# Performance work log

Hardware: AMD Instinct MI355X
Metric: run time of the kernel (lower is better)

Reference implementation:

```python
import jax, jax.numpy as jnp
import numpy as np

B, T, I, H = 64, 512, 512, 1024

def setup_inputs() -> dict:
    key = jax.random.key(0)
    ks = jax.random.split(key, 12)
    s_i = 1.0 / np.sqrt(I)
    s_h = 1.0 / np.sqrt(H)
    inp = {
        'x': jax.random.normal(ks[0], (B, T, I), dtype=jnp.float32),
        'h0': jnp.zeros((B, H), dtype=jnp.float32),
        'Wz': jax.random.uniform(ks[1], (H, I), jnp.float32, -s_i, s_i),
        'bz': jax.random.uniform(ks[2], (H,), jnp.float32, -s_i, s_i),
        'Uz': jax.random.uniform(ks[3], (H, H), jnp.float32, -s_h, s_h),
        'Wr': jax.random.uniform(ks[4], (H, I), jnp.float32, -s_i, s_i),
        'br': jax.random.uniform(ks[5], (H,), jnp.float32, -s_i, s_i),
        'Ur': jax.random.uniform(ks[6], (H, H), jnp.float32, -s_h, s_h),
        'Wh': jax.random.uniform(ks[7], (H, I), jnp.float32, -s_i, s_i),
        'bh': jax.random.uniform(ks[8], (H,), jnp.float32, -s_i, s_i),
        'Uh': jax.random.uniform(ks[9], (H, H), jnp.float32, -s_h, s_h),
    }
    return inp

def reference(x, h0, Wz, bz, Uz, Wr, br, Ur, Wh, bh, Uh):
    # Precompute all input projections for every timestep in 3 big GEMMs
    xz = jnp.einsum('bti,hi->bth', x, Wz) + bz  # [B,T,H]
    xr = jnp.einsum('bti,hi->bth', x, Wr) + br
    xh = jnp.einsum('bti,hi->bth', x, Wh) + bh
    # scan over time (recurrence)
    xs = (jnp.swapaxes(xz, 0, 1), jnp.swapaxes(xr, 0, 1), jnp.swapaxes(xh, 0, 1))  # [T,B,H]

    def step(h, inp):
        xz_t, xr_t, xh_t = inp
        z = jax.nn.sigmoid(xz_t + h @ Uz.T)
        r = jax.nn.sigmoid(xr_t + h @ Ur.T)
        h_tilde = jnp.tanh(xh_t + (r * h) @ Uh.T)
        h_new = (1.0 - z) * h + z * h_tilde
        return h_new, h_new

    h_last, outs = jax.lax.scan(step, h0, xs)  # outs: [T,B,H]
    outputs = jnp.swapaxes(outs, 0, 1)  # [B,T,H]
    return outputs, h_last
```

## Files before the change

kernel.cpp:

```cpp
#include <hip/hip_runtime.h>
#include <hip/hip_bf16.h>
#include <stdint.h>


#define B_ 64
#define T_ 512
#define I_ 512
#define H_ 1024

typedef __attribute__((ext_vector_type(4))) float f32x4;
typedef __attribute__((ext_vector_type(8))) short s16x8;

__device__ __forceinline__ unsigned short f2bf(float f) {
  union { float f; uint32_t u; } v; v.f = f;
  uint32_t u = v.u;
  u += 0x7fffu + ((u >> 16) & 1u);
  return (unsigned short)(u >> 16);
}
__device__ __forceinline__ float bf2f(unsigned short h) {
  union { uint32_t u; float f; } v; v.u = ((uint32_t)h) << 16;
  return v.f;
}

__global__ void k_split(const float* __restrict__ src, uint16_t* __restrict__ dst,
                        int kshift, int total) {
  int K = 1 << kshift;
  for (int i = blockIdx.x * blockDim.x + threadIdx.x; i < total;
       i += gridDim.x * blockDim.x) {
    int n = i >> kshift, k = i & (K - 1);
    float f = src[i];
    unsigned short hi = f2bf(f);
    unsigned short lo = f2bf(f - bf2f(hi));
    size_t base = (size_t)n * (3 * K);
    dst[base + k] = hi;
    dst[base + K + k] = lo;
    dst[base + 2 * K + k] = hi;
  }
}

__global__ void k_init(const float* __restrict__ h0, float* __restrict__ h,
                       uint16_t* __restrict__ h2) {
  for (int i = blockIdx.x * blockDim.x + threadIdx.x; i < B_ * H_;
       i += gridDim.x * blockDim.x) {
    float f = h0[i];
    h[i] = f;
    int b = i >> 10, j = i & 1023;
    unsigned short hi = f2bf(f);
    h2[b * 2048 + j] = hi;
    h2[b * 2048 + 1024 + j] = f2bf(f - bf2f(hi));
  }
}

__global__ __launch_bounds__(256) void k_proj(
    const float* __restrict__ x, const uint16_t* __restrict__ W2,
    const float* __restrict__ bz, const float* __restrict__ br,
    const float* __restrict__ bh,
    float* __restrict__ XP, int t0, int Tc, int MT) {
  __shared__ uint16_t As[128][72];
  __shared__ uint16_t Bs[128][72];
  int bid = blockIdx.x;
  int mt = bid % MT, nt = bid / MT;
  int tid = threadIdx.x;
  int w = tid >> 6, l = tid & 63;
  int wm = w >> 1, wn = w & 1;
  int lr = l & 15, lg = l >> 4;

  int gr[4], gc8[4];
  const float* asrc[4];
  const uint16_t* bsrc[4];
#pragma unroll
  for (int g = 0; g < 4; ++g) {
    int gran = tid + 256 * g;
    int r = gran >> 3, c8 = gran & 7;
    gr[g] = r; gc8[g] = c8;
    int n = mt * 128 + r;
    int b = n / Tc, tt = n % Tc;
    asrc[g] = x + ((size_t)b * T_ + (t0 + tt)) * I_;
    bsrc[g] = W2 + (size_t)(nt * 128 + r) * 1536;
  }

  f32x4 acc[4][4];
#pragma unroll
  for (int mi = 0; mi < 4; ++mi)
#pragma unroll
    for (int ni = 0; ni < 4; ++ni) {
      acc[mi][ni][0] = 0.f; acc[mi][ni][1] = 0.f;
      acc[mi][ni][2] = 0.f; acc[mi][ni][3] = 0.f;
    }

  float4 pa[8];
  uint4 pb[4];
#pragma unroll
  for (int g = 0; g < 4; ++g) {
    int kp = gc8[g] * 8;
    int xc = kp & 511;
    pa[2 * g] = *(const float4*)(asrc[g] + xc);
    pa[2 * g + 1] = *(const float4*)(asrc[g] + xc + 4);
    pb[g] = *(const uint4*)(bsrc[g] + kp);
  }

  for (int it = 0; it < 24; ++it) {
    __syncthreads();
    {
      int k0 = it * 64;
#pragma unroll
      for (int g = 0; g < 4; ++g) {
        int kp = k0 + gc8[g] * 8;
        bool lofl = (kp >= 1024);
        const float* pf = (const float*)&pa[2 * g];
        s16x8 v;
#pragma unroll
        for (int j = 0; j < 8; ++j) {
          float f = pf[j];
          unsigned short hi = f2bf(f);
          v[j] = (short)(lofl ? f2bf(f - bf2f(hi)) : hi);
        }
        *(s16x8*)(&As[gr[g]][gc8[g] * 8]) = v;
        *(uint4*)(&Bs[gr[g]][gc8[g] * 8]) = pb[g];
      }
    }
    if (it + 1 < 24) {
      int k0 = (it + 1) * 64;
#pragma unroll
      for (int g = 0; g < 4; ++g) {
        int kp = k0 + gc8[g] * 8;
        int xc = kp & 511;
        pa[2 * g] = *(const float4*)(asrc[g] + xc);
        pa[2 * g + 1] = *(const float4*)(asrc[g] + xc + 4);
        pb[g] = *(const uint4*)(bsrc[g] + kp);
      }
    }
    __syncthreads();
#pragma unroll
    for (int kk = 0; kk < 64; kk += 32) {
      s16x8 af[4], bf[4];
#pragma unroll
      for (int mi = 0; mi < 4; ++mi)
        af[mi] = *(const s16x8*)(&As[wm * 64 + mi * 16 + lr][kk + lg * 8]);
#pragma unroll
      for (int ni = 0; ni < 4; ++ni)
        bf[ni] = *(const s16x8*)(&Bs[wn * 64 + ni * 16 + lr][kk + lg * 8]);
#pragma unroll
      for (int mi = 0; mi < 4; ++mi)
#pragma unroll
        for (int ni = 0; ni < 4; ++ni)
          acc[mi][ni] = __builtin_amdgcn_mfma_f32_16x16x32_bf16(
              af[mi], bf[ni], acc[mi][ni], 0, 0, 0);
    }
  }

  int g_ = (nt * 128) >> 10;
  const float* bias = (g_ == 0) ? bz : ((g_ == 1) ? br : bh);
#pragma unroll
  for (int ni = 0; ni < 4; ++ni) {
    int col = nt * 128 + wn * 64 + ni * 16 + lr;
    int jc = col & 1023;
    float bv = bias[jc];
#pragma unroll
    for (int mi = 0; mi < 4; ++mi) {
      int nrow = mt * 128 + wm * 64 + mi * 16 + lg * 4;
      int b = nrow / Tc, tt = nrow % Tc;
#pragma unroll
      for (int v = 0; v < 4; ++v) {
        XP[((size_t)((tt * 3 + g_) * 64 + b)) * 1024 + jc] = acc[mi][ni][v] + bv;
        if (++tt == Tc) { tt = 0; ++b; }
      }
    }
  }
}

__global__ __launch_bounds__(512) void k_phase1(
    const uint16_t* __restrict__ h2, const uint16_t* __restrict__ U2,
    const float* __restrict__ XP, int tt,
    const float* __restrict__ h, float* __restrict__ zbuf,
    uint16_t* __restrict__ s2) {
  __shared__ float red[8][64][16];
  int tid = threadIdx.x, w = tid >> 6, l = tid & 63;
  int lr = l & 15, lg = l >> 4;
  int bid = blockIdx.x;
  int strip = (bid & 7) * 16 + (bid >> 3);
  int n0 = strip * 16;
  int kbase = w * 384;

  f32x4 acc[4];
#pragma unroll
  for (int mi = 0; mi < 4; ++mi) {
    acc[mi][0] = 0.f; acc[mi][1] = 0.f; acc[mi][2] = 0.f; acc[mi][3] = 0.f;
  }
  const uint16_t* brow = U2 + (size_t)(n0 + lr) * 3072;
#pragma unroll 4
  for (int ks = 0; ks < 12; ++ks) {
    int kp = kbase + ks * 32 + lg * 8;
    int ac = (kp < 1024) ? kp : kp - 1024;
    s16x8 bfv = *(const s16x8*)(brow + kp);
#pragma unroll
    for (int mi = 0; mi < 4; ++mi) {
      s16x8 afv = *(const s16x8*)(h2 + (size_t)(lr + 16 * mi) * 2048 + ac);
      acc[mi] = __builtin_amdgcn_mfma_f32_16x16x32_bf16(afv, bfv, acc[mi], 0, 0, 0);
    }
  }
#pragma unroll
  for (int mi = 0; mi < 4; ++mi)
#pragma unroll
    for (int v = 0; v < 4; ++v)
      red[w][mi * 16 + lg * 4 + v][lr] = acc[mi][v];
  __syncthreads();
  for (int e = tid; e < 1024; e += 512) {
    int b = e >> 4, c = e & 15;
    float s = 0.f;
#pragma unroll
    for (int q = 0; q < 8; ++q) s += red[q][b][c];
    int n = n0 + c;
    if (n < 1024) {
      float pre = s + XP[((size_t)(tt * 3 + 0) * 64 + b) * 1024 + n];
      zbuf[b * 1024 + n] = 1.f / (1.f + __expf(-pre));
    } else {
      int j = n - 1024;
      float pre = s + XP[((size_t)(tt * 3 + 1) * 64 + b) * 1024 + j];
      float r = 1.f / (1.f + __expf(-pre));
      float sv = r * h[b * 1024 + j];
      unsigned short hi = f2bf(sv);
      s2[b * 2048 + j] = hi;
      s2[b * 2048 + 1024 + j] = f2bf(sv - bf2f(hi));
    }
  }
}

__global__ __launch_bounds__(512) void k_phase2(
    const uint16_t* __restrict__ s2, const uint16_t* __restrict__ Uh2,
    const float* __restrict__ XP, int tt, int t,
    float* __restrict__ h, const float* __restrict__ zbuf,
    uint16_t* __restrict__ h2, float* __restrict__ out) {
  __shared__ float red[8][64][16];
  int tid = threadIdx.x, w = tid >> 6, l = tid & 63;
  int lr = l & 15, lg = l >> 4;
  int bid = blockIdx.x;
  int strip = (bid & 7) * 8 + (bid >> 3);
  int n0 = strip * 16;
  int kbase = w * 384;

  f32x4 acc[4];
#pragma unroll
  for (int mi = 0; mi < 4; ++mi) {
    acc[mi][0] = 0.f; acc[mi][1] = 0.f; acc[mi][2] = 0.f; acc[mi][3] = 0.f;
  }
  const uint16_t* brow = Uh2 + (size_t)(n0 + lr) * 3072;
#pragma unroll 4
  for (int ks = 0; ks < 12; ++ks) {
    int kp = kbase + ks * 32 + lg * 8;
    int ac = (kp < 1024) ? kp : kp - 1024;
    s16x8 bfv = *(const s16x8*)(brow + kp);
#pragma unroll
    for (int mi = 0; mi < 4; ++mi) {
      s16x8 afv = *(const s16x8*)(s2 + (size_t)(lr + 16 * mi) * 2048 + ac);
      acc[mi] = __builtin_amdgcn_mfma_f32_16x16x32_bf16(afv, bfv, acc[mi], 0, 0, 0);
    }
  }
#pragma unroll
  for (int mi = 0; mi < 4; ++mi)
#pragma unroll
    for (int v = 0; v < 4; ++v)
      red[w][mi * 16 + lg * 4 + v][lr] = acc[mi][v];
  __syncthreads();
  for (int e = tid; e < 1024; e += 512) {
    int b = e >> 4, c = e & 15;
    float s = 0.f;
#pragma unroll
    for (int q = 0; q < 8; ++q) s += red[q][b][c];
    int j = n0 + c;
    float pre = s + XP[((size_t)(tt * 3 + 2) * 64 + b) * 1024 + j];
    float ht = tanhf(pre);
    float z = zbuf[b * 1024 + j];
    float hv = h[b * 1024 + j];
    float hn = (1.f - z) * hv + z * ht;
    h[b * 1024 + j] = hn;
    unsigned short hi = f2bf(hn);
    h2[b * 2048 + j] = hi;
    h2[b * 2048 + 1024 + j] = f2bf(hn - bf2f(hi));
    out[((size_t)b * T_ + t) * 1024 + j] = hn;
    if (t == T_ - 1) out[(size_t)B_ * T_ * 1024 + b * 1024 + j] = hn;
  }
}

extern "C" void kernel_launch(void* const* d_in, const int* in_sizes, int n_in,
                              void* d_out, int out_size, void* d_ws, size_t ws_size,
                              hipStream_t stream) {
  const float* x  = (const float*)d_in[0];
  const float* h0 = (const float*)d_in[1];
  const float* Wz = (const float*)d_in[2];
  const float* bz = (const float*)d_in[3];
  const float* Uz = (const float*)d_in[4];
  const float* Wr = (const float*)d_in[5];
  const float* br = (const float*)d_in[6];
  const float* Ur = (const float*)d_in[7];
  const float* Wh = (const float*)d_in[8];
  const float* bh = (const float*)d_in[9];
  const float* Uh = (const float*)d_in[10];
  float* out = (float*)d_out;

  uint8_t* ws = (uint8_t*)d_ws;
  uint16_t* Uzr2 = (uint16_t*)(ws + 0);
  uint16_t* Uh2  = (uint16_t*)(ws + 12582912);
  uint16_t* W2   = (uint16_t*)(ws + 18874368);
  float*    hbuf = (float*)   (ws + 28311552);
  uint16_t* h2   = (uint16_t*)(ws + 28573696);
  uint16_t* s2   = (uint16_t*)(ws + 28835840);
  float*    zbuf = (float*)   (ws + 29097984);
  float*    XP   = (float*)   (ws + 29360128);

  size_t avail = (ws_size > 29360128u) ? (ws_size - 29360128u) : 0u;
  long long tcl = (long long)(avail / 786432u);
  int Tc = (tcl > 512) ? 512 : (int)tcl;
  Tc &= ~1;
  if (Tc < 2) Tc = 2;

  k_split<<<512, 256, 0, stream>>>(Uz, Uzr2, 10, 1024 * 1024);
  k_split<<<512, 256, 0, stream>>>(Ur, Uzr2 + (size_t)1024 * 3072, 10, 1024 * 1024);
  k_split<<<512, 256, 0, stream>>>(Uh, Uh2, 10, 1024 * 1024);
  k_split<<<512, 256, 0, stream>>>(Wz, W2, 9, 1024 * 512);
  k_split<<<512, 256, 0, stream>>>(Wr, W2 + (size_t)1024 * 1536, 9, 1024 * 512);
  k_split<<<512, 256, 0, stream>>>(Wh, W2 + (size_t)2048 * 1536, 9, 1024 * 512);
  k_init<<<64, 256, 0, stream>>>(h0, hbuf, h2);

  for (int t0 = 0; t0 < T_; t0 += Tc) {
    int Tcc = (Tc < T_ - t0) ? Tc : (T_ - t0);
    int MT = (B_ * Tcc) / 128;
    k_proj<<<MT * 24, 256, 0, stream>>>(x, W2, bz, br, bh, XP, t0, Tcc, MT);
    for (int tt = 0; tt < Tcc; ++tt) {
      k_phase1<<<128, 512, 0, stream>>>(h2, Uzr2, XP, tt, hbuf, zbuf, s2);
      k_phase2<<<64, 512, 0, stream>>>(s2, Uh2, XP, tt, t0 + tt, hbuf, zbuf, h2, out);
    }
  }
}
```

Baseline: 19.48 ms.

## Fuse GRU recurrence into persistent cooperative kernel with grid barriers and LDS-resident weights

Replaces the per-timestep pair of phase kernel launches with one persistent cooperative kernel of 192 workgroups. Each workgroup loads its 16-row slice of the recurrent weights into LDS once, split into bf16 hi/lo with a swizzle, and two hierarchical bucketed grid barriers separate the phases of each step. This removes about a thousand kernel launches and the repeated global reads of the split weights. In exchange it adds spin-wait barrier latency and depends on all workgroups being co-resident, and the large LDS footprint limits occupancy.

```diff
diff --git a/kernel.cpp b/kernel.cpp
--- a/kernel.cpp
+++ b/kernel.cpp
@@ -7,6 +7,11 @@
 #define T_ 512
 #define I_ 512
 #define H_ 1024
+#define NWG_A 128
+#define NWG_B 64
+#define NWG 192
+#define NBUCK 16
+#define BUCK_SZ (NWG / NBUCK)
 
 typedef __attribute__((ext_vector_type(4))) float f32x4;
 typedef __attribute__((ext_vector_type(8))) short s16x8;
@@ -169,116 +174,235 @@
   }
 }
 
-__global__ __launch_bounds__(512) void k_phase1(
-    const uint16_t* __restrict__ h2, const uint16_t* __restrict__ U2,
-    const float* __restrict__ XP, int tt,
-    const float* __restrict__ h, float* __restrict__ zbuf,
-    uint16_t* __restrict__ s2) {
-  __shared__ float red[8][64][16];
-  int tid = threadIdx.x, w = tid >> 6, l = tid & 63;
-  int lr = l & 15, lg = l >> 4;
-  int bid = blockIdx.x;
-  int strip = (bid & 7) * 16 + (bid >> 3);
-  int n0 = strip * 16;
-  int kbase = w * 384;
-
-  f32x4 acc[4];
-#pragma unroll
-  for (int mi = 0; mi < 4; ++mi) {
-    acc[mi][0] = 0.f; acc[mi][1] = 0.f; acc[mi][2] = 0.f; acc[mi][3] = 0.f;
-  }
-  const uint16_t* brow = U2 + (size_t)(n0 + lr) * 3072;
-#pragma unroll 4
-  for (int ks = 0; ks < 12; ++ks) {
-    int kp = kbase + ks * 32 + lg * 8;
-    int ac = (kp < 1024) ? kp : kp - 1024;
-    s16x8 bfv = *(const s16x8*)(brow + kp);
-#pragma unroll
-    for (int mi = 0; mi < 4; ++mi) {
-      s16x8 afv = *(const s16x8*)(h2 + (size_t)(lr + 16 * mi) * 2048 + ac);
-      acc[mi] = __builtin_amdgcn_mfma_f32_16x16x32_bf16(afv, bfv, acc[mi], 0, 0, 0);
-    }
-  }
-#pragma unroll
-  for (int mi = 0; mi < 4; ++mi)
-#pragma unroll
-    for (int v = 0; v < 4; ++v)
-      red[w][mi * 16 + lg * 4 + v][lr] = acc[mi][v];
+__device__ __forceinline__ void gridbar(unsigned* bar) {
   __syncthreads();
-  for (int e = tid; e < 1024; e += 512) {
-    int b = e >> 4, c = e & 15;
-    float s = 0.f;
-#pragma unroll
-    for (int q = 0; q < 8; ++q) s += red[q][b][c];
-    int n = n0 + c;
-    if (n < 1024) {
-      float pre = s + XP[((size_t)(tt * 3 + 0) * 64 + b) * 1024 + n];
-      zbuf[b * 1024 + n] = 1.f / (1.f + __expf(-pre));
+  if (threadIdx.x == 0) {
+    unsigned* gen = bar + 544;
+    unsigned g = __hip_atomic_load(gen, __ATOMIC_RELAXED, __HIP_MEMORY_SCOPE_AGENT);
+    __threadfence();
+    unsigned* bucket = bar + (blockIdx.x & (NBUCK - 1)) * 32;
+    unsigned old = __hip_atomic_fetch_add(bucket, 1u, __ATOMIC_RELAXED,
+                                          __HIP_MEMORY_SCOPE_AGENT);
+    if (old == BUCK_SZ - 1) {
+      __hip_atomic_store(bucket, 0u, __ATOMIC_RELAXED, __HIP_MEMORY_SCOPE_AGENT);
+      unsigned rold = __hip_atomic_fetch_add(bar + 512, 1u, __ATOMIC_RELAXED,
+                                             __HIP_MEMORY_SCOPE_AGENT);
+      if (rold == NBUCK - 1) {
+        __hip_atomic_store(bar + 512, 0u, __ATOMIC_RELAXED, __HIP_MEMORY_SCOPE_AGENT);
+        __hip_atomic_fetch_add(gen, 1u, __ATOMIC_RELAXED, __HIP_MEMORY_SCOPE_AGENT);
+      }
+    }
+    while (__hip_atomic_load(gen, __ATOMIC_RELAXED, __HIP_MEMORY_SCOPE_AGENT) == g)
+      __builtin_amdgcn_s_sleep(2);
+    __threadfence();
+  }
+  __syncthreads();
+}
+
+__global__ __launch_bounds__(512) void k_recur(
+    const float* __restrict__ Uz, const float* __restrict__ Ur,
+    const float* __restrict__ Uh, const float* __restrict__ XP,
+    int t0, int Tcc, float* __restrict__ h, uint16_t* __restrict__ h2,
+    uint16_t* __restrict__ s2, float* __restrict__ zbuf,
+    float* __restrict__ out, unsigned* __restrict__ bar) {
+  __shared__ uint16_t Wl[16 * 3072];
+  __shared__ float red[8 * 64 * 17];
+
+  const int tid = threadIdx.x;
+  const int w = tid >> 6, l = tid & 63;
+  const int lr = l & 15, lg = l >> 4;
+  const int bid = blockIdx.x;
+  const bool isA = (bid < NWG_A);
+  const int tile = isA ? bid : (bid - NWG_A);
+  const int n0 = tile * 16;
+
+  const float* src = isA ? ((n0 < 1024) ? (Uz + (size_t)n0 * 1024)
+                                        : (Ur + (size_t)(n0 - 1024) * 1024))
+                         : (Uh + (size_t)n0 * 1024);
+  for (int i = tid; i < 2048; i += 512) {
+    int r = i >> 7;
+    int k8 = (i & 127) * 8;
+    const float* p = src + r * 1024 + k8;
+    s16x8 hi8, lo8;
+#pragma unroll
+    for (int j = 0; j < 8; ++j) {
+      float f = p[j];
+      unsigned short hb = f2bf(f);
+      hi8[j] = (short)hb;
+      lo8[j] = (short)f2bf(f - bf2f(hb));
+    }
+    uint8_t* rowp = (uint8_t*)Wl + r * 6144;
+    int swz = (r & 7) << 4;
+    *(s16x8*)(rowp + ((k8 * 2) ^ swz)) = hi8;
+    *(s16x8*)(rowp + (((1024 + k8) * 2) ^ swz)) = lo8;
+    *(s16x8*)(rowp + (((2048 + k8) * 2) ^ swz)) = hi8;
+  }
+  __syncthreads();
+
+  const int KB0 = w * 128;
+  const int bswz = (lr & 7) << 4;
+  const uint8_t* browp = (const uint8_t*)Wl + lr * 6144;
+
+  for (int tt = 0; tt < Tcc; ++tt) {
+    const int t = t0 + tt;
+    float xpre[2], hpre[2];
+    if (isA) {
+#pragma unroll
+      for (int u = 0; u < 2; ++u) {
+        int e = tid + u * 512;
+        int b = e >> 4, c = e & 15;
+        int n = n0 + c;
+        if (n < 1024) {
+          xpre[u] = XP[((size_t)(tt * 3 + 0) * 64 + b) * 1024 + n];
+          hpre[u] = 0.f;
+        } else {
+          xpre[u] = XP[((size_t)(tt * 3 + 1) * 64 + b) * 1024 + (n - 1024)];
+          hpre[u] = h[b * 1024 + (n - 1024)];
+        }
+      }
+      f32x4 acc[4];
+#pragma unroll
+      for (int mi = 0; mi < 4; ++mi) {
+        acc[mi][0] = 0.f; acc[mi][1] = 0.f; acc[mi][2] = 0.f; acc[mi][3] = 0.f;
+      }
+      s16x8 ah[4][4];
+#pragma unroll
+      for (int ks = 0; ks < 4; ++ks) {
+        int kp = KB0 + ks * 32 + lg * 8;
+        s16x8 bfv = *(const s16x8*)(browp + ((kp * 2) ^ bswz));
+#pragma unroll
+        for (int mi = 0; mi < 4; ++mi) {
+          ah[ks][mi] = *(const s16x8*)(h2 + (size_t)(lr + 16 * mi) * 2048 + kp);
+          acc[mi] = __builtin_amdgcn_mfma_f32_16x16x32_bf16(ah[ks][mi], bfv,
+                                                            acc[mi], 0, 0, 0);
+        }
+      }
+#pragma unroll
+      for (int ks = 0; ks < 4; ++ks) {
+        int kp = 1024 + KB0 + ks * 32 + lg * 8;
+        s16x8 bfv = *(const s16x8*)(browp + ((kp * 2) ^ bswz));
+#pragma unroll
+        for (int mi = 0; mi < 4; ++mi)
+          acc[mi] = __builtin_amdgcn_mfma_f32_16x16x32_bf16(ah[ks][mi], bfv,
+                                                            acc[mi], 0, 0, 0);
+      }
+#pragma unroll
+      for (int ks = 0; ks < 4; ++ks) {
+        int kp = 2048 + KB0 + ks * 32 + lg * 8;
+        int ac = kp - 1024;
+        s16x8 bfv = *(const s16x8*)(browp + ((kp * 2) ^ bswz));
+#pragma unroll
+        for (int mi = 0; mi < 4; ++mi) {
+          s16x8 af = *(const s16x8*)(h2 + (size_t)(lr + 16 * mi) * 2048 + ac);
+          acc[mi] = __builtin_amdgcn_mfma_f32_16x16x32_bf16(af, bfv,
+                                                            acc[mi], 0, 0, 0);
+        }
+      }
+#pragma unroll
+      for (int mi = 0; mi < 4; ++mi)
+#pragma unroll
+        for (int v = 0; v < 4; ++v)
+          red[(w * 64 + mi * 16 + lg * 4 + v) * 17 + lr] = acc[mi][v];
+      __syncthreads();
+#pragma unroll
+      for (int u = 0; u < 2; ++u) {
+        int e = tid + u * 512;
+        int b = e >> 4, c = e & 15;
+        float s = 0.f;
+#pragma unroll
+        for (int q = 0; q < 8; ++q) s += red[(q * 64 + b) * 17 + c];
+        int n = n0 + c;
+        if (n < 1024) {
+          float pre = s + xpre[u];
+          zbuf[b * 1024 + n] = 1.f / (1.f + __expf(-pre));
+        } else {
+          int j = n - 1024;
+          float pre = s + xpre[u];
+          float r = 1.f / (1.f + __expf(-pre));
+          float sv = r * hpre[u];
+          unsigned short hb = f2bf(sv);
+          s2[b * 2048 + j] = hb;
+          s2[b * 2048 + 1024 + j] = f2bf(sv - bf2f(hb));
+        }
+      }
     } else {
-      int j = n - 1024;
-      float pre = s + XP[((size_t)(tt * 3 + 1) * 64 + b) * 1024 + j];
-      float r = 1.f / (1.f + __expf(-pre));
-      float sv = r * h[b * 1024 + j];
-      unsigned short hi = f2bf(sv);
-      s2[b * 2048 + j] = hi;
-      s2[b * 2048 + 1024 + j] = f2bf(sv - bf2f(hi));
-    }
-  }
-}
-
-__global__ __launch_bounds__(512) void k_phase2(
-    const uint16_t* __restrict__ s2, const uint16_t* __restrict__ Uh2,
-    const float* __restrict__ XP, int tt, int t,
-    float* __restrict__ h, const float* __restrict__ zbuf,
-    uint16_t* __restrict__ h2, float* __restrict__ out) {
-  __shared__ float red[8][64][16];
-  int tid = threadIdx.x, w = tid >> 6, l = tid & 63;
-  int lr = l & 15, lg = l >> 4;
-  int bid = blockIdx.x;
-  int strip = (bid & 7) * 8 + (bid >> 3);
-  int n0 = strip * 16;
-  int kbase = w * 384;
-
-  f32x4 acc[4];
-#pragma unroll
-  for (int mi = 0; mi < 4; ++mi) {
-    acc[mi][0] = 0.f; acc[mi][1] = 0.f; acc[mi][2] = 0.f; acc[mi][3] = 0.f;
-  }
-  const uint16_t* brow = Uh2 + (size_t)(n0 + lr) * 3072;
-#pragma unroll 4
-  for (int ks = 0; ks < 12; ++ks) {
-    int kp = kbase + ks * 32 + lg * 8;
-    int ac = (kp < 1024) ? kp : kp - 1024;
-    s16x8 bfv = *(const s16x8*)(brow + kp);
-#pragma unroll
-    for (int mi = 0; mi < 4; ++mi) {
-      s16x8 afv = *(const s16x8*)(s2 + (size_t)(lr + 16 * mi) * 2048 + ac);
-      acc[mi] = __builtin_amdgcn_mfma_f32_16x16x32_bf16(afv, bfv, acc[mi], 0, 0, 0);
-    }
-  }
-#pragma unroll
-  for (int mi = 0; mi < 4; ++mi)
-#pragma unroll
-    for (int v = 0; v < 4; ++v)
-      red[w][mi * 16 + lg * 4 + v][lr] = acc[mi][v];
-  __syncthreads();
-  for (int e = tid; e < 1024; e += 512) {
-    int b = e >> 4, c = e & 15;
-    float s = 0.f;
-#pragma unroll
-    for (int q = 0; q < 8; ++q) s += red[q][b][c];
-    int j = n0 + c;
-    float pre = s + XP[((size_t)(tt * 3 + 2) * 64 + b) * 1024 + j];
-    float ht = tanhf(pre);
-    float z = zbuf[b * 1024 + j];
-    float hv = h[b * 1024 + j];
-    float hn = (1.f - z) * hv + z * ht;
-    h[b * 1024 + j] = hn;
-    unsigned short hi = f2bf(hn);
-    h2[b * 2048 + j] = hi;
-    h2[b * 2048 + 1024 + j] = f2bf(hn - bf2f(hi));
-    out[((size_t)b * T_ + t) * 1024 + j] = hn;
-    if (t == T_ - 1) out[(size_t)B_ * T_ * 1024 + b * 1024 + j] = hn;
+#pragma unroll
+      for (int u = 0; u < 2; ++u) {
+        int e = tid + u * 512;
+        int b = e >> 4, c = e & 15;
+        int j = n0 + c;
+        xpre[u] = XP[((size_t)(tt * 3 + 2) * 64 + b) * 1024 + j];
+        hpre[u] = h[b * 1024 + j];
+      }
+    }
+    gridbar(bar);
+    if (!isA) {
+      f32x4 acc[4];
+#pragma unroll
+      for (int mi = 0; mi < 4; ++mi) {
+        acc[mi][0] = 0.f; acc[mi][1] = 0.f; acc[mi][2] = 0.f; acc[mi][3] = 0.f;
+      }
+      s16x8 ah[4][4];
+#pragma unroll
+      for (int ks = 0; ks < 4; ++ks) {
+        int kp = KB0 + ks * 32 + lg * 8;
+        s16x8 bfv = *(const s16x8*)(browp + ((kp * 2) ^ bswz));
+#pragma unroll
+        for (int mi = 0; mi < 4; ++mi) {
+          ah[ks][mi] = *(const s16x8*)(s2 + (size_t)(lr + 16 * mi) * 2048 + kp);
+          acc[mi] = __builtin_amdgcn_mfma_f32_16x16x32_bf16(ah[ks][mi], bfv,
+                                                            acc[mi], 0, 0, 0);
+        }
+      }
+#pragma unroll
+      for (int ks = 0; ks < 4; ++ks) {
+        int kp = 1024 + KB0 + ks * 32 + lg * 8;
+        s16x8 bfv = *(const s16x8*)(browp + ((kp * 2) ^ bswz));
+#pragma unroll
+        for (int mi = 0; mi < 4; ++mi)
+          acc[mi] = __builtin_amdgcn_mfma_f32_16x16x32_bf16(ah[ks][mi], bfv,
+                                                            acc[mi], 0, 0, 0);
+      }
+#pragma unroll
+      for (int ks = 0; ks < 4; ++ks) {
+        int kp = 2048 + KB0 + ks * 32 + lg * 8;
+        int ac = kp - 1024;
+        s16x8 bfv = *(const s16x8*)(browp + ((kp * 2) ^ bswz));
+#pragma unroll
+        for (int mi = 0; mi < 4; ++mi) {
+          s16x8 af = *(const s16x8*)(s2 + (size_t)(lr + 16 * mi) * 2048 + ac);
+          acc[mi] = __builtin_amdgcn_mfma_f32_16x16x32_bf16(af, bfv,
+                                                            acc[mi], 0, 0, 0);
+        }
+      }
+#pragma unroll
+      for (int mi = 0; mi < 4; ++mi)
+#pragma unroll
+        for (int v = 0; v < 4; ++v)
+          red[(w * 64 + mi * 16 + lg * 4 + v) * 17 + lr] = acc[mi][v];
+      __syncthreads();
+#pragma unroll
+      for (int u = 0; u < 2; ++u) {
+        int e = tid + u * 512;
+        int b = e >> 4, c = e & 15;
+        float s = 0.f;
+#pragma unroll
+        for (int q = 0; q < 8; ++q) s += red[(q * 64 + b) * 17 + c];
+        int j = n0 + c;
+        float pre = s + xpre[u];
+        float ht = tanhf(pre);
+        float z = zbuf[b * 1024 + j];
+        float hv = hpre[u];
+        float hn = (1.f - z) * hv + z * ht;
+        h[b * 1024 + j] = hn;
+        unsigned short hb = f2bf(hn);
+        h2[b * 2048 + j] = hb;
+        h2[b * 2048 + 1024 + j] = f2bf(hn - bf2f(hb));
+        out[((size_t)b * T_ + t) * 1024 + j] = hn;
+        if (t == T_ - 1) out[(size_t)B_ * T_ * 1024 + b * 1024 + j] = hn;
+      }
+    }
+    gridbar(bar);
   }
 }
 
@@ -299,36 +423,37 @@
   float* out = (float*)d_out;
 
   uint8_t* ws = (uint8_t*)d_ws;
-  uint16_t* Uzr2 = (uint16_t*)(ws + 0);
-  uint16_t* Uh2  = (uint16_t*)(ws + 12582912);
-  uint16_t* W2   = (uint16_t*)(ws + 18874368);
-  float*    hbuf = (float*)   (ws + 28311552);
-  uint16_t* h2   = (uint16_t*)(ws + 28573696);
-  uint16_t* s2   = (uint16_t*)(ws + 28835840);
-  float*    zbuf = (float*)   (ws + 29097984);
-  float*    XP   = (float*)   (ws + 29360128);
-
-  size_t avail = (ws_size > 29360128u) ? (ws_size - 29360128u) : 0u;
+  uint16_t* W2   = (uint16_t*)(ws + 0);
+  float*    hbuf = (float*)   (ws + 9437184);
+  uint16_t* h2   = (uint16_t*)(ws + 9699328);
+  uint16_t* s2   = (uint16_t*)(ws + 9961472);
+  float*    zbuf = (float*)   (ws + 10223616);
+  unsigned* bar  = (unsigned*)(ws + 10485760);
+  float*    XP   = (float*)   (ws + 10489856);
+
+  hipMemsetAsync(bar, 0, 4096, stream);
+
+  k_split<<<512, 256, 0, stream>>>(Wz, W2, 9, 1024 * 512);
+  k_split<<<512, 256, 0, stream>>>(Wr, W2 + (size_t)1024 * 1536, 9, 1024 * 512);
+  k_split<<<512, 256, 0, stream>>>(Wh, W2 + (size_t)2048 * 1536, 9, 1024 * 512);
+  k_init<<<64, 256, 0, stream>>>(h0, hbuf, h2);
+
+  size_t avail = (ws_size > 10489856u) ? (ws_size - 10489856u) : 0u;
   long long tcl = (long long)(avail / 786432u);
   int Tc = (tcl > 512) ? 512 : (int)tcl;
   Tc &= ~1;
   if (Tc < 2) Tc = 2;
 
-  k_split<<<512, 256, 0, stream>>>(Uz, Uzr2, 10, 1024 * 1024);
-  k_split<<<512, 256, 0, stream>>>(Ur, Uzr2 + (size_t)1024 * 3072, 10, 1024 * 1024);
-  k_split<<<512, 256, 0, stream>>>(Uh, Uh2, 10, 1024 * 1024);
-  k_split<<<512, 256, 0, stream>>>(Wz, W2, 9, 1024 * 512);
-  k_split<<<512, 256, 0, stream>>>(Wr, W2 + (size_t)1024 * 1536, 9, 1024 * 512);
-  k_split<<<512, 256, 0, stream>>>(Wh, W2 + (size_t)2048 * 1536, 9, 1024 * 512);
-  k_init<<<64, 256, 0, stream>>>(h0, hbuf, h2);
-
   for (int t0 = 0; t0 < T_; t0 += Tc) {
     int Tcc = (Tc < T_ - t0) ? Tc : (T_ - t0);
     int MT = (B_ * Tcc) / 128;
     k_proj<<<MT * 24, 256, 0, stream>>>(x, W2, bz, br, bh, XP, t0, Tcc, MT);
-    for (int tt = 0; tt < Tcc; ++tt) {
-      k_phase1<<<128, 512, 0, stream>>>(h2, Uzr2, XP, tt, hbuf, zbuf, s2);
-      k_phase2<<<64, 512, 0, stream>>>(s2, Uh2, XP, tt, t0 + tt, hbuf, zbuf, h2, out);
-    }
-  }
-}
+
+    int t0v = t0, tccv = Tcc;
+    void* args[] = {(void*)&Uz, (void*)&Ur, (void*)&Uh, (void*)&XP,
+                    (void*)&t0v, (void*)&tccv, (void*)&hbuf, (void*)&h2,
+                    (void*)&s2, (void*)&zbuf, (void*)&out, (void*)&bar};
+    hipLaunchCooperativeKernel((void*)k_recur, dim3(NWG), dim3(512),
+                               args, 0, stream);
+  }
+}
```

Result: slower. 20.00 ms (+2.6%).
